# Optimization experiments

Measured on AMD Instinct MI355X. Metric: run time of the kernel, lower is better.

The kernel has to match this reference:

```python
import jax, jax.numpy as jnp
import numpy as np

_ALIAS = {11: 11, 13: 11, 16: 11, 21: 21, 22: 21, 23: 21, 31: 31, 32: 31, 33: 31,
          41: 41, 42: 41, 43: 41, 44: 41, 51: 51, 52: 51, 53: 51}
_COMPAT = {11: (11, 13, 16), 21: (14, 15, 21, 22, 23), 31: (15, 31, 32, 33),
           41: (41, 42, 43, 44), 51: (15, 51, 52, 53)}
_VOCAB = 64


def _tables():
    alias = np.full((_VOCAB,), -1, np.int32)
    for k, v in _ALIAS.items():
        alias[k] = v
    compat = np.zeros((_VOCAB, _VOCAB), np.float32)
    has = np.zeros((_VOCAB,), np.bool_)
    for r, toks in _COMPAT.items():
        has[r] = True
        for t in toks:
            compat[r, t] = 1.0
    return jnp.asarray(alias), jnp.asarray(compat), jnp.asarray(has)


def setup_inputs() -> dict:
    key = jax.random.key(0)
    k1, k2, k3, k4 = jax.random.split(key, 4)
    B, T, D, A, S, TTL = 8, 4096, 1024, 32, 16, 64
    H = max(TTL * 4, S * 4)
    hidden = jax.random.normal(k1, (B, T, D), jnp.float32)
    anchor_repr = jax.random.normal(k2, (B, A, D), jnp.float32)
    input_ids = jax.random.randint(k3, (B, T), 0, _VOCAB, jnp.int32)
    # end_idx in [S-1, T-H) so span start >= 0 and full horizon fits in T
    anchor_end = jax.random.randint(k4, (B, A), S - 1, T - H, jnp.int32)
    return {"hidden": hidden, "anchor_repr": anchor_repr, "input_ids": input_ids,
            "anchor_end": anchor_end, "span_len": S, "ttl": TTL}


def reference(hidden, anchor_repr, input_ids, anchor_end, span_len, ttl):
    alias_t, compat_t, has_t = _tables()
    B, T, D = hidden.shape
    A = anchor_end.shape[1]
    S = int(span_len)
    H = max(int(ttl) * 4, S * 4)
    W = H - S + 1
    eps = 1e-8

    bidx = jnp.arange(B)[:, None, None]
    start = anchor_end + 1                                   # [B,A]
    fut_idx = start[..., None] + jnp.arange(H)               # [B,A,H]
    future = hidden[bidx, fut_idx]                           # [B,A,H,D]
    fut_tok = input_ids[bidx, fut_idx]                       # [B,A,H]
    span_idx = (anchor_end - S + 1)[..., None] + jnp.arange(S)
    span = input_ids[bidx, span_idx]                         # [B,A,S]
    anchor_tok = input_ids[jnp.arange(B)[:, None], anchor_end]  # [B,A]

    # hidden-space stats (cosine_similarity with F.cosine_similarity eps)
    mean_future = future.mean(axis=2)                        # [B,A,D]
    nr = jnp.maximum(jnp.linalg.norm(anchor_repr, axis=-1), eps)
    nf = jnp.maximum(jnp.linalg.norm(mean_future, axis=-1), eps)
    sim = (anchor_repr * mean_future).sum(-1) / (nr * nf)    # [B,A]
    future_shift = jnp.linalg.norm(future - anchor_repr[:, :, None, :], axis=-1).mean(-1)
    hidden_c = jnp.maximum(0.0, (1.0 - sim) / 2.0)
    token_c = 1.0 - (fut_tok == anchor_tok[..., None]).astype(jnp.float32).mean(-1)

    # sliding windows over the horizon
    win_idx = jnp.arange(W)[:, None] + jnp.arange(S)[None, :]  # [W,S]
    win = fut_tok[:, :, win_idx]                               # [B,A,W,S]
    eq = (win == span[:, :, None, :]).astype(jnp.float32)     # [B,A,W,S]
    exact = eq.mean(-1)                                       # [B,A,W]
    pos_w = jnp.linspace(1.0, 0.4, S)
    pos_w = pos_w / pos_w.sum()
    positional = (eq * pos_w).sum(-1)

    # set-overlap: count distinct anchor tokens present in window
    eqmat = span[..., :, None] == span[..., None, :]          # [B,A,S,S]
    tri = jnp.tril(jnp.ones((S, S), bool), -1)
    first_occ = ~(eqmat & tri).any(-1)                        # first occurrence mask
    first_f = first_occ.astype(jnp.float32)
    denom = first_f.sum(-1)                                   # |set(anchor_span)|
    in_win = (win[..., :, None] == span[:, :, None, None, :]).any(-2)  # [B,A,W,S]
    overlap = (in_win.astype(jnp.float32) * first_f[:, :, None, :]).sum(-1) / denom[:, :, None]

    # infer_reference_root: first aliased token, else mode (smallest on ties)
    alias_span = alias_t[span]                                # [B,A,S], -1 if no alias
    has_a = alias_span >= 0
    first_i = jnp.argmax(has_a, -1)
    first_root = jnp.take_along_axis(alias_span, first_i[..., None], -1)[..., 0]
    counts = eqmat.sum(-1)
    maxc = counts.max(-1, keepdims=True)
    mode = jnp.where(counts == maxc, span, _VOCAB).min(-1)
    root = jnp.where(has_a.any(-1), first_root, mode)         # [B,A]

    r4 = root[:, :, None, None]
    root_pers = (win == r4).astype(jnp.float32).mean(-1)      # [B,A,W]
    alias_c = (alias_t[win] == r4).astype(jnp.float32).mean(-1)
    hard = compat_t[r4, win].mean(-1)
    regime = jnp.where(has_t[root][:, :, None],
                       0.55 * hard + 0.2 * overlap + 0.15 * alias_c + 0.1 * root_pers,
                       0.45 * exact + 0.3 * overlap + 0.1 * alias_c + 0.15 * root_pers)

    sims = 0.25 * exact + 0.15 * overlap + 0.35 * positional + 0.25 * regime
    best = sims.max(-1)
    mrp = root_pers.mean(-1)
    mrc = regime.mean(-1)
    dmass = (sims >= 0.6).astype(jnp.float32).mean(-1)
    dcoh = 0.6 * sims.mean(-1) + 0.25 * mrp + 0.15 * mrc
    pattern_c = 1.0 - (0.6 * best + 0.2 * mrp + 0.2 * mrc)

    contr = jnp.clip(0.2 * hidden_c + 0.2 * token_c + 0.6 * pattern_c, 0.0, 1.0)
    # [8,B,A]: contradiction, future_shift, similarity, hidden_c, token_c, pattern_c, mass, coherence
    return jnp.stack([contr, future_shift, sim, hidden_c, token_c, pattern_c, dmass, dcoh], 0)
```

## Files before the change

### kernel.cpp

```cpp
#include <hip/hip_runtime.h>
#include <math.h>

constexpr int kB = 8;
constexpr int kT = 4096;
constexpr int kD = 1024;
constexpr int kA = 32;
constexpr int kS = 16;
constexpr int kH = 256;
constexpr int kW = kH - kS + 1;
constexpr int kBA = kB * kA;
constexpr int kRB = 128;
constexpr int kNJ = kT / kRB;
constexpr int kMK = 3;
constexpr int NC = kD / 256;

constexpr int NT = 1024;
constexpr int NW = NT / 64;

__device__ inline float wredsum(float v) {
#pragma unroll
    for (int m = 32; m >= 1; m >>= 1) v += __shfl_xor(v, m, 64);
    return v;
}
__device__ inline float wredmax(float v) {
#pragma unroll
    for (int m = 32; m >= 1; m >>= 1) v = fmaxf(v, __shfl_xor(v, m, 64));
    return v;
}

__device__ inline int alias_of(int t) {
    switch (t) {
        case 11: case 13: case 16: return 11;
        case 21: case 22: case 23: return 21;
        case 31: case 32: case 33: return 31;
        case 41: case 42: case 43: case 44: return 41;
        case 51: case 52: case 53: return 51;
        default: return -1;
    }
}

__global__ __launch_bounds__(NT) void s1_kernel(
    const float* __restrict__ hidden,
    const float* __restrict__ anchor_repr,
    const int*   __restrict__ anchor_end,
    float*       __restrict__ partial,
    float*       __restrict__ pshift)
{
    __shared__ float lanc[8][kD];
    __shared__ float comb[NW][kD];
    __shared__ float ssh[NW];

    const int id = blockIdx.x;
    const int b  = id & 7;
    const int j  = id >> 3;
    const int tid  = threadIdx.x;
    const int lane = tid & 63;
    const int wave = tid >> 6;
    const int g  = wave >> 3;
    const int ww = wave & 7;
    const int r0 = j * kRB;

    const int* ae = anchor_end + b * kA;
    unsigned mask = 0;
    for (int a = 0; a < kA; ++a) {
        int st = ae[a] + 1;
        if ((st >> 7) <= j && j <= ((st + kH - 1) >> 7)) mask |= 1u << a;
    }

    const float* hbase = hidden + ((size_t)(b * kT + r0)) * kD + 4 * lane;

    while (mask) {
        int aidx[8], stv[8];
        int npass = 0;
        unsigned rem = mask;
#pragma unroll
        for (int s = 0; s < 8; ++s) {
            if (rem) { aidx[s] = __ffs((int)rem) - 1; rem &= rem - 1u; ++npass; }
            else       aidx[s] = -1;
            stv[s] = (aidx[s] >= 0) ? (ae[aidx[s]] + 1) : 0x40000000;
        }
        mask = rem;

#pragma unroll
        for (int s = 0; s < 8; ++s)
            if (aidx[s] >= 0)
                lanc[s][tid] = anchor_repr[((size_t)(b * kA + aidx[s])) * kD + tid];
        __syncthreads();

        int stc[4];
#pragma unroll
        for (int c = 0; c < 4; ++c) stc[c] = g ? stv[2 * c + 1] : stv[2 * c];

        float4 vs[4][NC];
#pragma unroll
        for (int c = 0; c < 4; ++c)
#pragma unroll
            for (int ch = 0; ch < NC; ++ch) vs[c][ch] = make_float4(0.f, 0.f, 0.f, 0.f);
        float sacc[4] = {0.f, 0.f, 0.f, 0.f};

        for (int t = 0; t < kRB / 8; ++t) {
            const int lr = ww + 8 * t;
            const int r  = r0 + lr;
            const bool in0 = ((unsigned)(r - stc[0]) < (unsigned)kH);
            const bool in1 = ((unsigned)(r - stc[1]) < (unsigned)kH);
            const bool in2 = ((unsigned)(r - stc[2]) < (unsigned)kH);
            const bool in3 = ((unsigned)(r - stc[3]) < (unsigned)kH);
            if (!(in0 | in1 | in2 | in3)) continue;
            float4 x[NC];
#pragma unroll
            for (int ch = 0; ch < NC; ++ch)
                x[ch] = *(const float4*)(hbase + (size_t)lr * kD + 256 * ch);
            const bool inc[4] = {in0, in1, in2, in3};
#pragma unroll
            for (int c = 0; c < 4; ++c) {
                if (inc[c]) {
                    const float* ap = &lanc[2 * c + g][4 * lane];
                    float acc = 0.f;
#pragma unroll
                    for (int ch = 0; ch < NC; ++ch) {
                        float4 a4 = *(const float4*)(ap + 256 * ch);
                        vs[c][ch].x += x[ch].x; vs[c][ch].y += x[ch].y;
                        vs[c][ch].z += x[ch].z; vs[c][ch].w += x[ch].w;
                        float d0 = x[ch].x - a4.x, d1 = x[ch].y - a4.y;
                        float d2 = x[ch].z - a4.z, d3 = x[ch].w - a4.w;
                        acc += d0*d0 + d1*d1 + d2*d2 + d3*d3;
                    }
#pragma unroll
                    for (int m = 32; m >= 1; m >>= 1) acc += __shfl_xor(acc, m, 64);
                    sacc[c] += sqrtf(acc);
                }
            }
        }

#pragma unroll
        for (int c = 0; c < 4; ++c) {
            __syncthreads();
#pragma unroll
            for (int ch = 0; ch < NC; ++ch)
                *(float4*)&comb[wave][256 * ch + 4 * lane] = vs[c][ch];
            if (lane == 0) ssh[wave] = sacc[c];
            __syncthreads();
            float s0 = 0.f, s1 = 0.f;
#pragma unroll
            for (int w = 0; w < 8; ++w) { s0 += comb[w][tid]; s1 += comb[8 + w][tid]; }
            if (2 * c < npass) {
                const int ba0 = b * kA + aidx[2 * c];
                const int k0  = j - (stv[2 * c] >> 7);
                partial[((size_t)(ba0 * kMK + k0) << 10) + tid] = s0;
            }
            if (2 * c + 1 < npass) {
                const int ba1 = b * kA + aidx[2 * c + 1];
                const int k1  = j - (stv[2 * c + 1] >> 7);
                partial[((size_t)(ba1 * kMK + k1) << 10) + tid] = s1;
            }
            if (tid == 0 && 2 * c < npass) {
                float t0 = 0.f;
                for (int w = 0; w < 8; ++w) t0 += ssh[w];
                pshift[(b * kA + aidx[2 * c]) * kMK + (j - (stv[2 * c] >> 7))] = t0;
            }
            if (tid == 64 && 2 * c + 1 < npass) {
                float t1 = 0.f;
                for (int w = 8; w < 16; ++w) t1 += ssh[w];
                pshift[(b * kA + aidx[2 * c + 1]) * kMK + (j - (stv[2 * c + 1] >> 7))] = t1;
            }
        }
        __syncthreads();
    }
}

__global__ __launch_bounds__(NT) void s2_kernel(
    const float* __restrict__ anchor_repr,
    const int*   __restrict__ input_ids,
    const int*   __restrict__ anchor_end,
    const float* __restrict__ partial,
    const float* __restrict__ pshift,
    float*       __restrict__ out)
{
    __shared__ int   sfut[kH];
    __shared__ int   sspan[kS];
    __shared__ float sposw[kS];
    __shared__ float sr1[NW], sr2[NW], sr3[NW], sr4[NW], sr5[NW];
    __shared__ float s_sim, s_shift, s_hidc, s_tokc;
    __shared__ int   s_root, s_has;
    __shared__ unsigned long long s_spanmask, s_amask, s_hmask;
    __shared__ float s_denom;

    const int ba   = blockIdx.x;
    const int b    = ba / kA;
    const int tid  = threadIdx.x;
    const int lane = tid & 63;
    const int wave = tid >> 6;

    const int e     = anchor_end[ba];
    const int start = e + 1;
    const int* ids  = input_ids + b * kT;
    const int anchor_tok = ids[e];

    if (tid < kH) sfut[tid] = ids[start + tid];
    if (tid < kS) {
        sspan[tid] = ids[e - kS + 1 + tid];
        sposw[tid] = (1.0f - 0.04f * (float)tid) * (1.0f / 11.2f);
    }

    const float* arow = anchor_repr + (size_t)ba * kD;
    const int nk = ((start + kH - 1) >> 7) - (start >> 7) + 1;
    float tot = 0.f;
    for (int k = 0; k < nk; ++k)
        tot += partial[((size_t)(ba * kMK + k) << 10) + tid];
    float m  = tot * (1.0f / kH);
    float av = arow[tid];
    float pm2  = m * m;
    float pdot = m * av;
    float pa2  = av * av;
    float peq  = (tid < kH && sfut[tid] == anchor_tok) ? 1.f : 0.f;
    pm2 = wredsum(pm2); pdot = wredsum(pdot); pa2 = wredsum(pa2); peq = wredsum(peq);
    if (lane == 0) { sr2[wave] = pm2; sr3[wave] = pdot; sr4[wave] = pa2; sr5[wave] = peq; }
    __syncthreads();

    if (tid == 0) {
        float m2 = 0.f, dt = 0.f, a2 = 0.f, eqc = 0.f;
        for (int w = 0; w < NW; ++w) { m2 += sr2[w]; dt += sr3[w]; a2 += sr4[w]; eqc += sr5[w]; }
        float shift = 0.f;
        for (int k = 0; k < nk; ++k) shift += pshift[ba * kMK + k];
        float nf = fmaxf(sqrtf(m2), 1e-8f);
        float nr = fmaxf(sqrtf(a2), 1e-8f);
        float sim = dt / (nr * nf);
        s_sim   = sim;
        s_shift = shift * (1.0f / kH);
        s_hidc  = fmaxf(0.f, (1.f - sim) * 0.5f);
        s_tokc  = 1.f - eqc * (1.0f / kH);
    }
    if (tid == 64) {
        unsigned long long spanmask = 0;
        for (int s = 0; s < kS; ++s) spanmask |= 1ull << sspan[s];
        int root = -1;
        for (int s = 0; s < kS; ++s) { int al = alias_of(sspan[s]); if (al >= 0) { root = al; break; } }
        if (root < 0) {
            int counts[kS], maxc = 0;
            for (int s = 0; s < kS; ++s) {
                int c = 0;
                for (int s2 = 0; s2 < kS; ++s2) c += (sspan[s2] == sspan[s]) ? 1 : 0;
                counts[s] = c; if (c > maxc) maxc = c;
            }
            int mode = 64;
            for (int s = 0; s < kS; ++s) if (counts[s] == maxc && sspan[s] < mode) mode = sspan[s];
            root = mode;
        }
        unsigned long long am = 0, hm = 0; int has = 0;
        switch (root) {
            case 11: am = (1ull<<11)|(1ull<<13)|(1ull<<16);            hm = am;                       has = 1; break;
            case 21: am = (1ull<<21)|(1ull<<22)|(1ull<<23);            hm = am|(1ull<<14)|(1ull<<15); has = 1; break;
            case 31: am = (1ull<<31)|(1ull<<32)|(1ull<<33);            hm = am|(1ull<<15);            has = 1; break;
            case 41: am = (1ull<<41)|(1ull<<42)|(1ull<<43)|(1ull<<44); hm = am;                       has = 1; break;
            case 51: am = (1ull<<51)|(1ull<<52)|(1ull<<53);            hm = am|(1ull<<15);            has = 1; break;
            default: break;
        }
        s_root = root; s_has = has; s_spanmask = spanmask; s_amask = am; s_hmask = hm;
        s_denom = (float)__popcll(spanmask);
    }
    __syncthreads();

    const int root = s_root, has = s_has;
    const unsigned long long spanmask = s_spanmask, amask = s_amask, hmask = s_hmask;
    const float inv_denom = 1.0f / s_denom;

    float sims = -1e30f, rootpers = 0.f, regime = 0.f, simsum = 0.f, cnt = 0.f;
    if (tid < kW) {
        float wex = 0.f, wpos = 0.f, wrp = 0.f, wal = 0.f, whard = 0.f;
        unsigned long long wm = 0;
#pragma unroll
        for (int s = 0; s < kS; ++s) {
            int tok = sfut[tid + s];
            wm |= 1ull << tok;
            bool eq = (tok == sspan[s]);
            wex  += eq ? 1.f : 0.f;
            wpos += eq ? sposw[s] : 0.f;
            wrp  += (tok == root) ? 1.f : 0.f;
            wal  += ((amask >> tok) & 1ull) ? 1.f : 0.f;
            whard += ((hmask >> tok) & 1ull) ? 1.f : 0.f;
        }
        float exact  = wex * (1.f / kS);
        float overlap = (float)__popcll(wm & spanmask) * inv_denom;
        rootpers = wrp * (1.f / kS);
        float aliasc = wal * (1.f / kS);
        float hard   = whard * (1.f / kS);
        regime = has ? (0.55f*hard  + 0.2f*overlap + 0.15f*aliasc + 0.1f*rootpers)
                     : (0.45f*exact + 0.3f*overlap + 0.1f*aliasc  + 0.15f*rootpers);
        sims = 0.25f*exact + 0.15f*overlap + 0.35f*wpos + 0.25f*regime;
        simsum = sims;
        cnt = (sims >= 0.6f) ? 1.f : 0.f;
    }
    float rmax = wredmax(sims);
    float rsum = wredsum(simsum);
    float rrp  = wredsum(rootpers);
    float rreg = wredsum(regime);
    float rcnt = wredsum(cnt);
    if (lane == 0) { sr1[wave] = rmax; sr2[wave] = rsum; sr3[wave] = rrp; sr4[wave] = rreg; sr5[wave] = rcnt; }
    __syncthreads();

    if (tid == 0) {
        float best = -1e30f, ssum = 0.f, srp = 0.f, sreg = 0.f, scnt = 0.f;
        for (int w = 0; w < NW; ++w) {
            best = fmaxf(best, sr1[w]); ssum += sr2[w]; srp += sr3[w]; sreg += sr4[w]; scnt += sr5[w];
        }
        const float invW = 1.0f / (float)kW;
        float msims = ssum * invW, mrp = srp * invW, mrc = sreg * invW, dmass = scnt * invW;
        float dcoh      = 0.6f*msims + 0.25f*mrp + 0.15f*mrc;
        float pattern_c = 1.f - (0.6f*best + 0.2f*mrp + 0.2f*mrc);
        float contr     = 0.2f*s_hidc + 0.2f*s_tokc + 0.6f*pattern_c;
        contr = fminf(fmaxf(contr, 0.f), 1.f);
        const int n = kB * kA;
        out[0*n + ba] = contr;
        out[1*n + ba] = s_shift;
        out[2*n + ba] = s_sim;
        out[3*n + ba] = s_hidc;
        out[4*n + ba] = s_tokc;
        out[5*n + ba] = pattern_c;
        out[6*n + ba] = dmass;
        out[7*n + ba] = dcoh;
    }
}

__global__ __launch_bounds__(NT) void monitor_kernel(
    const float* __restrict__ hidden,
    const float* __restrict__ anchor_repr,
    const int*   __restrict__ input_ids,
    const int*   __restrict__ anchor_end,
    float*       __restrict__ out)
{
    __shared__ float smean[NW][kD];
    __shared__ int   sfut[kH];
    __shared__ int   sspan[kS];
    __shared__ float sposw[kS];
    __shared__ float sr1[NW], sr2[NW], sr3[NW], sr4[NW], sr5[NW];
    __shared__ float s_sim, s_shift, s_hidc, s_tokc;
    __shared__ int   s_root, s_has;
    __shared__ unsigned long long s_spanmask, s_amask, s_hmask;
    __shared__ float s_denom;

    const int id = blockIdx.x;
    const int ba = (id & 7) * 32 + (id >> 3);
    const int b  = ba / kA;
    const int tid  = threadIdx.x;
    const int lane = tid & 63;
    const int wave = tid >> 6;

    const int e     = anchor_end[ba];
    const int start = e + 1;
    const int* ids  = input_ids + b * kT;
    const int anchor_tok = ids[e];

    if (tid < kH) sfut[tid] = ids[start + tid];
    if (tid < kS) {
        sspan[tid] = ids[e - kS + 1 + tid];
        sposw[tid] = (1.0f - 0.04f * (float)tid) * (1.0f / 11.2f);
    }

    const float* arow = anchor_repr + (size_t)ba * kD;
    float4 anc[NC];
#pragma unroll
    for (int c = 0; c < NC; ++c) anc[c] = *(const float4*)(arow + 256 * c + 4 * lane);
    const float* hbase = hidden + ((size_t)b * kT + start) * kD + 4 * lane;

    float sum[NC][4];
#pragma unroll
    for (int c = 0; c < NC; ++c)
#pragma unroll
        for (int j = 0; j < 4; ++j) sum[c][j] = 0.f;

    float ss[kH / NW];
#pragma unroll
    for (int k = 0; k < kH / NW; ++k) ss[k] = 0.f;
#pragma unroll
    for (int k = 0; k < kH / NW; ++k) {
        const float* rp = hbase + (size_t)(wave + NW * k) * kD;
        float acc = 0.f;
#pragma unroll
        for (int c = 0; c < NC; ++c) {
            float4 x = *(const float4*)(rp + 256 * c);
            float4 a = anc[c];
            sum[c][0] += x.x; sum[c][1] += x.y; sum[c][2] += x.z; sum[c][3] += x.w;
            float d0 = x.x - a.x, d1 = x.y - a.y, d2 = x.z - a.z, d3 = x.w - a.w;
            acc += d0*d0 + d1*d1 + d2*d2 + d3*d3;
        }
        ss[k] = acc;
    }
#pragma unroll
    for (int m = 32; m >= 1; m >>= 1) {
#pragma unroll
        for (int k = 0; k < kH / NW; ++k) ss[k] += __shfl_xor(ss[k], m, 64);
    }
    float shift_acc = 0.f;
#pragma unroll
    for (int k = 0; k < kH / NW; ++k) shift_acc += sqrtf(ss[k]);

#pragma unroll
    for (int c = 0; c < NC; ++c)
        *(float4*)&smean[wave][256 * c + 4 * lane] =
            make_float4(sum[c][0], sum[c][1], sum[c][2], sum[c][3]);
    if (lane == 0) sr1[wave] = shift_acc;
    __syncthreads();

    float tot = 0.f;
#pragma unroll
    for (int w = 0; w < NW; ++w) tot += smean[w][tid];
    float m  = tot * (1.0f / kH);
    float av = arow[tid];
    float pm2  = m * m;
    float pdot = m * av;
    float pa2  = av * av;
    float peq  = (tid < kH && sfut[tid] == anchor_tok) ? 1.f : 0.f;
    pm2 = wredsum(pm2); pdot = wredsum(pdot); pa2 = wredsum(pa2); peq = wredsum(peq);
    if (lane == 0) { sr2[wave] = pm2; sr3[wave] = pdot; sr4[wave] = pa2; sr5[wave] = peq; }
    __syncthreads();

    if (tid == 0) {
        float shift = 0.f, m2 = 0.f, dt = 0.f, a2 = 0.f, eqc = 0.f;
        for (int w = 0; w < NW; ++w) {
            shift += sr1[w]; m2 += sr2[w]; dt += sr3[w]; a2 += sr4[w]; eqc += sr5[w];
        }
        float nf = fmaxf(sqrtf(m2), 1e-8f);
        float nr = fmaxf(sqrtf(a2), 1e-8f);
        float sim = dt / (nr * nf);
        s_sim   = sim;
        s_shift = shift * (1.0f / kH);
        s_hidc  = fmaxf(0.f, (1.f - sim) * 0.5f);
        s_tokc  = 1.f - eqc * (1.0f / kH);
    }
    if (tid == 64) {
        unsigned long long spanmask = 0;
        for (int s = 0; s < kS; ++s) spanmask |= 1ull << sspan[s];
        int root = -1;
        for (int s = 0; s < kS; ++s) { int al = alias_of(sspan[s]); if (al >= 0) { root = al; break; } }
        if (root < 0) {
            int counts[kS], maxc = 0;
            for (int s = 0; s < kS; ++s) {
                int c = 0;
                for (int s2 = 0; s2 < kS; ++s2) c += (sspan[s2] == sspan[s]) ? 1 : 0;
                counts[s] = c; if (c > maxc) maxc = c;
            }
            int mode = 64;
            for (int s = 0; s < kS; ++s) if (counts[s] == maxc && sspan[s] < mode) mode = sspan[s];
            root = mode;
        }
        unsigned long long am = 0, hm = 0; int has = 0;
        switch (root) {
            case 11: am = (1ull<<11)|(1ull<<13)|(1ull<<16);            hm = am;                       has = 1; break;
            case 21: am = (1ull<<21)|(1ull<<22)|(1ull<<23);            hm = am|(1ull<<14)|(1ull<<15); has = 1; break;
            case 31: am = (1ull<<31)|(1ull<<32)|(1ull<<33);            hm = am|(1ull<<15);            has = 1; break;
            case 41: am = (1ull<<41)|(1ull<<42)|(1ull<<43)|(1ull<<44); hm = am;                       has = 1; break;
            case 51: am = (1ull<<51)|(1ull<<52)|(1ull<<53);            hm = am|(1ull<<15);            has = 1; break;
            default: break;
        }
        s_root = root; s_has = has; s_spanmask = spanmask; s_amask = am; s_hmask = hm;
        s_denom = (float)__popcll(spanmask);
    }
    __syncthreads();

    const int root = s_root, has = s_has;
    const unsigned long long spanmask = s_spanmask, amask = s_amask, hmask = s_hmask;
    const float inv_denom = 1.0f / s_denom;

    float sims = -1e30f, rootpers = 0.f, regime = 0.f, simsum = 0.f, cnt = 0.f;
    if (tid < kW) {
        float wex = 0.f, wpos = 0.f, wrp = 0.f, wal = 0.f, whard = 0.f;
        unsigned long long wm = 0;
#pragma unroll
        for (int s = 0; s < kS; ++s) {
            int tok = sfut[tid + s];
            wm |= 1ull << tok;
            bool eq = (tok == sspan[s]);
            wex  += eq ? 1.f : 0.f;
            wpos += eq ? sposw[s] : 0.f;
            wrp  += (tok == root) ? 1.f : 0.f;
            wal  += ((amask >> tok) & 1ull) ? 1.f : 0.f;
            whard += ((hmask >> tok) & 1ull) ? 1.f : 0.f;
        }
        float exact  = wex * (1.f / kS);
        float overlap = (float)__popcll(wm & spanmask) * inv_denom;
        rootpers = wrp * (1.f / kS);
        float aliasc = wal * (1.f / kS);
        float hard   = whard * (1.f / kS);
        regime = has ? (0.55f*hard  + 0.2f*overlap + 0.15f*aliasc + 0.1f*rootpers)
                     : (0.45f*exact + 0.3f*overlap + 0.1f*aliasc  + 0.15f*rootpers);
        sims = 0.25f*exact + 0.15f*overlap + 0.35f*wpos + 0.25f*regime;
        simsum = sims;
        cnt = (sims >= 0.6f) ? 1.f : 0.f;
    }
    float rmax = wredmax(sims);
    float rsum = wredsum(simsum);
    float rrp  = wredsum(rootpers);
    float rreg = wredsum(regime);
    float rcnt = wredsum(cnt);
    if (lane == 0) { sr1[wave] = rmax; sr2[wave] = rsum; sr3[wave] = rrp; sr4[wave] = rreg; sr5[wave] = rcnt; }
    __syncthreads();

    if (tid == 0) {
        float best = -1e30f, ssum = 0.f, srp = 0.f, sreg = 0.f, scnt = 0.f;
        for (int w = 0; w < NW; ++w) {
            best = fmaxf(best, sr1[w]); ssum += sr2[w]; srp += sr3[w]; sreg += sr4[w]; scnt += sr5[w];
        }
        const float invW = 1.0f / (float)kW;
        float msims = ssum * invW, mrp = srp * invW, mrc = sreg * invW, dmass = scnt * invW;
        float dcoh      = 0.6f*msims + 0.25f*mrp + 0.15f*mrc;
        float pattern_c = 1.f - (0.6f*best + 0.2f*mrp + 0.2f*mrc);
        float contr     = 0.2f*s_hidc + 0.2f*s_tokc + 0.6f*pattern_c;
        contr = fminf(fmaxf(contr, 0.f), 1.f);
        const int n = kB * kA;
        out[0*n + ba] = contr;
        out[1*n + ba] = s_shift;
        out[2*n + ba] = s_sim;
        out[3*n + ba] = s_hidc;
        out[4*n + ba] = s_tokc;
        out[5*n + ba] = pattern_c;
        out[6*n + ba] = dmass;
        out[7*n + ba] = dcoh;
    }
}

extern "C" void kernel_launch(void* const* d_in, const int* in_sizes, int n_in,
                              void* d_out, int out_size, void* d_ws, size_t ws_size,
                              hipStream_t stream) {
    const float* hidden      = (const float*)d_in[0];
    const float* anchor_repr = (const float*)d_in[1];
    const int*   input_ids   = (const int*)d_in[2];
    const int*   anchor_end  = (const int*)d_in[3];
    float* out = (float*)d_out;

    const size_t n_partial = (size_t)kBA * kMK * kD;
    const size_t need      = (n_partial + kBA * kMK) * sizeof(float);

    if (d_ws != nullptr && ws_size >= need) {
        float* partial = (float*)d_ws;
        float* pshift  = partial + n_partial;
        hipLaunchKernelGGL(s1_kernel, dim3(kB * kNJ), dim3(NT), 0, stream,
                           hidden, anchor_repr, anchor_end, partial, pshift);
        hipLaunchKernelGGL(s2_kernel, dim3(kBA), dim3(NT), 0, stream,
                           anchor_repr, input_ids, anchor_end, partial, pshift, out);
    } else {
        hipLaunchKernelGGL(monitor_kernel, dim3(kBA), dim3(NT), 0, stream,
                           hidden, anchor_repr, input_ids, anchor_end, out);
    }
}
```

Before: 230.2 us.

## Shrink stage-one row chunks to 64 and keep anchor vectors in registers

Stage one now uses 64-row chunks with 512-thread blocks and occupancy hint 4, so there are twice as many, smaller blocks. Each wave owns 8 contiguous rows and processes two anchors per pass, holding their vectors in registers instead of staging eight anchors in shared memory. Per-row distance reductions are batched across rows before the sqrt, and blocks with no overlapping anchors exit early. The partial-sum slot count grows to 5 and stage two gains a missing barrier, at the cost of more partial traffic and more re-reads of hidden rows when several anchors overlap a chunk.

```diff
diff --git a/kernel.cpp b/kernel.cpp
--- a/kernel.cpp
+++ b/kernel.cpp
@@ -9,10 +9,14 @@
 constexpr int kH = 256;
 constexpr int kW = kH - kS + 1;
 constexpr int kBA = kB * kA;
-constexpr int kRB = 128;
-constexpr int kNJ = kT / kRB;
-constexpr int kMK = 3;
 constexpr int NC = kD / 256;
+
+constexpr int CH   = 64;
+constexpr int NCH  = kT / CH;
+constexpr int NT1  = 512;
+constexpr int NW1  = NT1 / 64;
+constexpr int RW   = CH / NW1;
+constexpr int kMK  = 5;
 
 constexpr int NT = 1024;
 constexpr int NW = NT / 64;
@@ -39,132 +43,147 @@
     }
 }
 
-__global__ __launch_bounds__(NT) void s1_kernel(
+__global__ __launch_bounds__(NT1, 4) void s1_kernel(
     const float* __restrict__ hidden,
     const float* __restrict__ anchor_repr,
     const int*   __restrict__ anchor_end,
     float*       __restrict__ partial,
     float*       __restrict__ pshift)
 {
-    __shared__ float lanc[8][kD];
-    __shared__ float comb[NW][kD];
-    __shared__ float ssh[NW];
-
-    const int id = blockIdx.x;
-    const int b  = id & 7;
-    const int j  = id >> 3;
+    __shared__ float comb[NW1][kD];
+    __shared__ float ssh[NW1];
+
+    const int b = blockIdx.x & 7;
+    const int j = blockIdx.x >> 3;
     const int tid  = threadIdx.x;
     const int lane = tid & 63;
     const int wave = tid >> 6;
-    const int g  = wave >> 3;
-    const int ww = wave & 7;
-    const int r0 = j * kRB;
-
+    const int r0 = j * CH;
     const int* ae = anchor_end + b * kA;
+
     unsigned mask = 0;
     for (int a = 0; a < kA; ++a) {
         int st = ae[a] + 1;
-        if ((st >> 7) <= j && j <= ((st + kH - 1) >> 7)) mask |= 1u << a;
-    }
-
-    const float* hbase = hidden + ((size_t)(b * kT + r0)) * kD + 4 * lane;
+        int head = st >> 6, tail = (st + kH - 1) >> 6;
+        if (head <= j && j <= tail) mask |= 1u << a;
+    }
+    if (!mask) return;
+
+    const int rw0 = r0 + wave * RW;
+    const float* hbase = hidden + ((size_t)(b * kT + rw0)) * kD + 4 * lane;
 
     while (mask) {
-        int aidx[8], stv[8];
-        int npass = 0;
-        unsigned rem = mask;
-#pragma unroll
-        for (int s = 0; s < 8; ++s) {
-            if (rem) { aidx[s] = __ffs((int)rem) - 1; rem &= rem - 1u; ++npass; }
-            else       aidx[s] = -1;
-            stv[s] = (aidx[s] >= 0) ? (ae[aidx[s]] + 1) : 0x40000000;
-        }
-        mask = rem;
-
-#pragma unroll
-        for (int s = 0; s < 8; ++s)
-            if (aidx[s] >= 0)
-                lanc[s][tid] = anchor_repr[((size_t)(b * kA + aidx[s])) * kD + tid];
+        const int c0 = __ffs((int)mask) - 1; mask &= mask - 1u;
+        const int c1 = mask ? (__ffs((int)mask) - 1) : -1;
+        if (c1 >= 0) mask &= mask - 1u;
+        const int st0 = ae[c0] + 1;
+        const int st1 = (c1 >= 0) ? (ae[c1] + 1) : 0x40000000;
+
+        const float* a0p = anchor_repr + ((size_t)(b * kA + c0)) * kD + 4 * lane;
+        const float* a1p = anchor_repr + ((size_t)(b * kA + (c1 >= 0 ? c1 : c0))) * kD + 4 * lane;
+        float4 A0[NC], A1[NC];
+#pragma unroll
+        for (int c = 0; c < NC; ++c) {
+            A0[c] = *(const float4*)(a0p + 256 * c);
+            A1[c] = *(const float4*)(a1p + 256 * c);
+        }
+
+        float4 vs0[NC], vs1[NC];
+#pragma unroll
+        for (int c = 0; c < NC; ++c) {
+            vs0[c] = make_float4(0.f, 0.f, 0.f, 0.f);
+            vs1[c] = make_float4(0.f, 0.f, 0.f, 0.f);
+        }
+        float q0[RW], q1[RW];
+#pragma unroll
+        for (int t = 0; t < RW; ++t) { q0[t] = 0.f; q1[t] = 0.f; }
+
+#pragma unroll
+        for (int t = 0; t < RW; ++t) {
+            const int r = rw0 + t;
+            const bool in0 = ((unsigned)(r - st0) < (unsigned)kH);
+            const bool in1 = ((unsigned)(r - st1) < (unsigned)kH);
+            if (!(in0 | in1)) continue;
+            float4 x[NC];
+#pragma unroll
+            for (int c = 0; c < NC; ++c)
+                x[c] = *(const float4*)(hbase + (size_t)t * kD + 256 * c);
+            if (in0) {
+                float acc = 0.f;
+#pragma unroll
+                for (int c = 0; c < NC; ++c) {
+                    vs0[c].x += x[c].x; vs0[c].y += x[c].y;
+                    vs0[c].z += x[c].z; vs0[c].w += x[c].w;
+                    float d0 = x[c].x - A0[c].x, d1 = x[c].y - A0[c].y;
+                    float d2 = x[c].z - A0[c].z, d3 = x[c].w - A0[c].w;
+                    acc += d0*d0 + d1*d1 + d2*d2 + d3*d3;
+                }
+                q0[t] = acc;
+            }
+            if (in1) {
+                float acc = 0.f;
+#pragma unroll
+                for (int c = 0; c < NC; ++c) {
+                    vs1[c].x += x[c].x; vs1[c].y += x[c].y;
+                    vs1[c].z += x[c].z; vs1[c].w += x[c].w;
+                    float d0 = x[c].x - A1[c].x, d1 = x[c].y - A1[c].y;
+                    float d2 = x[c].z - A1[c].z, d3 = x[c].w - A1[c].w;
+                    acc += d0*d0 + d1*d1 + d2*d2 + d3*d3;
+                }
+                q1[t] = acc;
+            }
+        }
+
+#pragma unroll
+        for (int m = 32; m >= 1; m >>= 1) {
+#pragma unroll
+            for (int t = 0; t < RW; ++t) {
+                q0[t] += __shfl_xor(q0[t], m, 64);
+                q1[t] += __shfl_xor(q1[t], m, 64);
+            }
+        }
+        float sa0 = 0.f, sa1 = 0.f;
+#pragma unroll
+        for (int t = 0; t < RW; ++t) { sa0 += sqrtf(q0[t]); sa1 += sqrtf(q1[t]); }
+
         __syncthreads();
-
-        int stc[4];
-#pragma unroll
-        for (int c = 0; c < 4; ++c) stc[c] = g ? stv[2 * c + 1] : stv[2 * c];
-
-        float4 vs[4][NC];
-#pragma unroll
-        for (int c = 0; c < 4; ++c)
-#pragma unroll
-            for (int ch = 0; ch < NC; ++ch) vs[c][ch] = make_float4(0.f, 0.f, 0.f, 0.f);
-        float sacc[4] = {0.f, 0.f, 0.f, 0.f};
-
-        for (int t = 0; t < kRB / 8; ++t) {
-            const int lr = ww + 8 * t;
-            const int r  = r0 + lr;
-            const bool in0 = ((unsigned)(r - stc[0]) < (unsigned)kH);
-            const bool in1 = ((unsigned)(r - stc[1]) < (unsigned)kH);
-            const bool in2 = ((unsigned)(r - stc[2]) < (unsigned)kH);
-            const bool in3 = ((unsigned)(r - stc[3]) < (unsigned)kH);
-            if (!(in0 | in1 | in2 | in3)) continue;
-            float4 x[NC];
-#pragma unroll
-            for (int ch = 0; ch < NC; ++ch)
-                x[ch] = *(const float4*)(hbase + (size_t)lr * kD + 256 * ch);
-            const bool inc[4] = {in0, in1, in2, in3};
-#pragma unroll
-            for (int c = 0; c < 4; ++c) {
-                if (inc[c]) {
-                    const float* ap = &lanc[2 * c + g][4 * lane];
-                    float acc = 0.f;
-#pragma unroll
-                    for (int ch = 0; ch < NC; ++ch) {
-                        float4 a4 = *(const float4*)(ap + 256 * ch);
-                        vs[c][ch].x += x[ch].x; vs[c][ch].y += x[ch].y;
-                        vs[c][ch].z += x[ch].z; vs[c][ch].w += x[ch].w;
-                        float d0 = x[ch].x - a4.x, d1 = x[ch].y - a4.y;
-                        float d2 = x[ch].z - a4.z, d3 = x[ch].w - a4.w;
-                        acc += d0*d0 + d1*d1 + d2*d2 + d3*d3;
-                    }
-#pragma unroll
-                    for (int m = 32; m >= 1; m >>= 1) acc += __shfl_xor(acc, m, 64);
-                    sacc[c] += sqrtf(acc);
-                }
-            }
-        }
-
-#pragma unroll
-        for (int c = 0; c < 4; ++c) {
+#pragma unroll
+        for (int c = 0; c < NC; ++c)
+            *(float4*)&comb[wave][256 * c + 4 * lane] = vs0[c];
+        if (lane == 0) ssh[wave] = sa0;
+        __syncthreads();
+        {
+            const int slot = (b * kA + c0) * kMK + (j - (st0 >> 6));
+            float s_lo = 0.f, s_hi = 0.f;
+#pragma unroll
+            for (int w = 0; w < NW1; ++w) { s_lo += comb[w][tid]; s_hi += comb[w][tid + NT1]; }
+            partial[((size_t)slot << 10) + tid]       = s_lo;
+            partial[((size_t)slot << 10) + tid + NT1] = s_hi;
+            if (tid == 0) {
+                float s = 0.f;
+                for (int w = 0; w < NW1; ++w) s += ssh[w];
+                pshift[slot] = s;
+            }
+        }
+        if (c1 >= 0) {
             __syncthreads();
 #pragma unroll
-            for (int ch = 0; ch < NC; ++ch)
-                *(float4*)&comb[wave][256 * ch + 4 * lane] = vs[c][ch];
-            if (lane == 0) ssh[wave] = sacc[c];
+            for (int c = 0; c < NC; ++c)
+                *(float4*)&comb[wave][256 * c + 4 * lane] = vs1[c];
+            if (lane == 0) ssh[wave] = sa1;
             __syncthreads();
-            float s0 = 0.f, s1 = 0.f;
-#pragma unroll
-            for (int w = 0; w < 8; ++w) { s0 += comb[w][tid]; s1 += comb[8 + w][tid]; }
-            if (2 * c < npass) {
-                const int ba0 = b * kA + aidx[2 * c];
-                const int k0  = j - (stv[2 * c] >> 7);
-                partial[((size_t)(ba0 * kMK + k0) << 10) + tid] = s0;
-            }
-            if (2 * c + 1 < npass) {
-                const int ba1 = b * kA + aidx[2 * c + 1];
-                const int k1  = j - (stv[2 * c + 1] >> 7);
-                partial[((size_t)(ba1 * kMK + k1) << 10) + tid] = s1;
-            }
-            if (tid == 0 && 2 * c < npass) {
-                float t0 = 0.f;
-                for (int w = 0; w < 8; ++w) t0 += ssh[w];
-                pshift[(b * kA + aidx[2 * c]) * kMK + (j - (stv[2 * c] >> 7))] = t0;
-            }
-            if (tid == 64 && 2 * c + 1 < npass) {
-                float t1 = 0.f;
-                for (int w = 8; w < 16; ++w) t1 += ssh[w];
-                pshift[(b * kA + aidx[2 * c + 1]) * kMK + (j - (stv[2 * c + 1] >> 7))] = t1;
-            }
-        }
-        __syncthreads();
+            const int slot = (b * kA + c1) * kMK + (j - (st1 >> 6));
+            float s_lo = 0.f, s_hi = 0.f;
+#pragma unroll
+            for (int w = 0; w < NW1; ++w) { s_lo += comb[w][tid]; s_hi += comb[w][tid + NT1]; }
+            partial[((size_t)slot << 10) + tid]       = s_lo;
+            partial[((size_t)slot << 10) + tid + NT1] = s_hi;
+            if (tid == 0) {
+                float s = 0.f;
+                for (int w = 0; w < NW1; ++w) s += ssh[w];
+                pshift[slot] = s;
+            }
+        }
     }
 }
 
@@ -201,9 +220,10 @@
         sspan[tid] = ids[e - kS + 1 + tid];
         sposw[tid] = (1.0f - 0.04f * (float)tid) * (1.0f / 11.2f);
     }
+    __syncthreads();
 
     const float* arow = anchor_repr + (size_t)ba * kD;
-    const int nk = ((start + kH - 1) >> 7) - (start >> 7) + 1;
+    const int nk = ((start + kH - 1) >> 6) - (start >> 6) + 1;
     float tot = 0.f;
     for (int k = 0; k < nk; ++k)
         tot += partial[((size_t)(ba * kMK + k) << 10) + tid];
@@ -533,7 +553,7 @@
     if (d_ws != nullptr && ws_size >= need) {
         float* partial = (float*)d_ws;
         float* pshift  = partial + n_partial;
-        hipLaunchKernelGGL(s1_kernel, dim3(kB * kNJ), dim3(NT), 0, stream,
+        hipLaunchKernelGGL(s1_kernel, dim3(kB * NCH), dim3(NT1), 0, stream,
                            hidden, anchor_repr, anchor_end, partial, pshift);
         hipLaunchKernelGGL(s2_kernel, dim3(kBA), dim3(NT), 0, stream,
                            anchor_repr, input_ids, anchor_end, partial, pshift, out);
```

Result: slower. 316.1 us (+37.3%).
